# Kernel tuning notes

Measured on AMD Instinct MI355X. Metric: run time of the kernel, lower is better.

## Reference

```python
import jax, jax.numpy as jnp
import numpy as np

WS = 16        # window size
SHIFT = 8      # shift for odd blocks
DEPTH = 2      # number of stacked blocks
HEADS = 8
EPS = 1e-5


def window_partition(x, ws):
    # x: (B,H,W,C) -> (B*nw, ws*ws, C)
    B, H, W, C = x.shape
    x = x.reshape(B, H // ws, ws, W // ws, ws, C).transpose(0, 1, 3, 2, 4, 5)
    return x.reshape(-1, ws * ws, C)


def window_reverse(wins, ws, H, W):
    B = wins.shape[0] // ((H // ws) * (W // ws))
    x = wins.reshape(B, H // ws, W // ws, ws, ws, -1).transpose(0, 1, 3, 2, 4, 5)
    return x.reshape(B, H, W, -1)


def layernorm(x, g, b):
    m = jnp.mean(x, axis=-1, keepdims=True)
    v = jnp.mean(jnp.square(x - m), axis=-1, keepdims=True)
    return (x - m) * jax.lax.rsqrt(v + EPS) * g + b


def _make_rpi(ws):
    # Swin relative position index, shape (ws*ws, ws*ws), int32
    coords = np.stack(np.meshgrid(np.arange(ws), np.arange(ws), indexing='ij'))  # (2,ws,ws)
    coords = coords.reshape(2, -1)
    rel = coords[:, :, None] - coords[:, None, :]  # (2, n, n)
    rel = rel + (ws - 1)
    rpi = rel[0] * (2 * ws - 1) + rel[1]
    return jnp.asarray(rpi, dtype=jnp.int32)


def _make_attn_mask(H, W, ws, shift):
    # Swin shifted-window mask, shape (nw, n, n) with 0 / -100
    img = np.zeros((1, H, W, 1), dtype=np.float32)
    cnt = 0
    slices = (slice(0, -ws), slice(-ws, -shift), slice(-shift, None))
    for hs in slices:
        for wsl in slices:
            img[:, hs, wsl, :] = cnt
            cnt += 1
    mw = window_partition(jnp.asarray(img), ws).reshape(-1, ws * ws)  # (nw, n)
    mask = mw[:, None, :] - mw[:, :, None]
    return jnp.where(mask != 0, jnp.float32(-100.0), jnp.float32(0.0))


def setup_inputs() -> dict:
    key = jax.random.key(0)
    ks = jax.random.split(key, 8)
    B, H, W, C = 8, 64, 64, 256
    hid = 4 * C
    d = DEPTH
    s = 0.02
    inp = {
        'x':      jax.random.normal(ks[0], (B, H, W, C), jnp.float32),
        'ln1_g':  jnp.ones((d, C), jnp.float32),
        'ln1_b':  jnp.zeros((d, C), jnp.float32),
        'qkv_w':  jax.random.normal(ks[1], (d, C, 3 * C), jnp.float32) * s,
        'qkv_b':  jnp.zeros((d, 3 * C), jnp.float32),
        'rpb':    jax.random.normal(ks[2], (d, (2 * WS - 1) ** 2, HEADS), jnp.float32) * s,
        'proj_w': jax.random.normal(ks[3], (d, C, C), jnp.float32) * s,
        'proj_b': jnp.zeros((d, C), jnp.float32),
        'ln2_g':  jnp.ones((d, C), jnp.float32),
        'ln2_b':  jnp.zeros((d, C), jnp.float32),
        'fc1_w':  jax.random.normal(ks[4], (d, C, hid), jnp.float32) * s,
        'fc1_b':  jnp.zeros((d, hid), jnp.float32),
        'fc2_w':  jax.random.normal(ks[5], (d, hid, C), jnp.float32) * s,
        'fc2_b':  jnp.zeros((d, C), jnp.float32),
        'attn_mask': _make_attn_mask(H, W, WS, SHIFT),
        'rpi':    _make_rpi(WS),
    }
    return inp


def _forward(x, ln1_g, ln1_b, qkv_w, qkv_b, rpb, proj_w, proj_b,
             ln2_g, ln2_b, fc1_w, fc1_b, fc2_w, fc2_b, attn_mask, rpi):
    B, H, W, C = x.shape
    n = WS * WS
    hd = C // HEADS
    scale = jnp.float32(hd) ** -0.5
    for i in range(DEPTH):
        shift = SHIFT if (i % 2 == 1) else 0
        shortcut = x
        y = layernorm(x, ln1_g[i], ln1_b[i])
        if shift:
            y = jnp.roll(y, (-shift, -shift), axis=(1, 2))
        wins = window_partition(y, WS)                      # (b_, n, C)
        b_ = wins.shape[0]
        qkv = wins @ qkv_w[i] + qkv_b[i]
        qkv = qkv.reshape(b_, n, 3, HEADS, hd).transpose(2, 0, 3, 1, 4)
        q, k, v = qkv[0] * scale, qkv[1], qkv[2]            # (b_,h,n,hd)
        attn = jnp.einsum('bhnd,bhmd->bhnm', q, k)          # (b_,h,n,n)
        bias = rpb[i][rpi.reshape(-1)].reshape(n, n, HEADS).transpose(2, 0, 1)
        attn = attn + bias[None]
        if shift:
            nw = attn_mask.shape[0]
            attn = attn.reshape(B, nw, HEADS, n, n) + attn_mask[None, :, None]
            attn = attn.reshape(b_, HEADS, n, n)
        attn = jax.nn.softmax(attn, axis=-1)
        out = jnp.einsum('bhnm,bhmd->bhnd', attn, v)
        out = out.transpose(0, 2, 1, 3).reshape(b_, n, C)
        out = out @ proj_w[i] + proj_b[i]
        y = window_reverse(out, WS, H, W)
        if shift:
            y = jnp.roll(y, (shift, shift), axis=(1, 2))
        x = shortcut + y
        z = layernorm(x, ln2_g[i], ln2_b[i])
        z = jax.nn.gelu(z @ fc1_w[i] + fc1_b[i], approximate=False)
        z = z @ fc2_w[i] + fc2_b[i]
        x = x + z
    return x


def reference(x, ln1_g, ln1_b, qkv_w, qkv_b, rpb, proj_w, proj_b,
              ln2_g, ln2_b, fc1_w, fc1_b, fc2_w, fc2_b, attn_mask, rpi):
    return _forward(x, ln1_g, ln1_b, qkv_w, qkv_b, rpb, proj_w, proj_b,
                    ln2_g, ln2_b, fc1_w, fc1_b, fc2_w, fc2_b, attn_mask, rpi)
```

## Files before the change

kernel.cpp:

```cpp
#include <hip/hip_runtime.h>

typedef unsigned short u16;
typedef __attribute__((ext_vector_type(8))) short short8;
typedef __attribute__((ext_vector_type(4))) float f32x4;

#define GLDS16(gp, sp) __builtin_amdgcn_global_load_lds( \
    (const __attribute__((address_space(1))) void*)(gp),  \
    (__attribute__((address_space(3))) void*)(sp), 16, 0, 0)

__device__ __forceinline__ u16 f2bf(float f) {
  union { float f; unsigned u; } x; x.f = f;
  unsigned r = (x.u + 0x7fffu + ((x.u >> 16) & 1u)) >> 16;
  return (u16)r;
}
__device__ __forceinline__ float bf2f(u16 v) {
  union { unsigned u; float f; } x; x.u = ((unsigned)v) << 16; return x.f;
}
__device__ __forceinline__ unsigned cvt_pk_bf16(float lo, float hi) {
  unsigned r;
  asm("v_cvt_pk_bf16_f32 %0, %1, %2" : "=v"(r) : "v"(lo), "v"(hi));
  return r;
}
__device__ __forceinline__ float gelu_t(float v) {
  float i = v * (1.f + 0.044715f * v * v);
  float e = __expf(-1.5957691216057308f * i);
  return v * __builtin_amdgcn_rcpf(1.f + e);
}

__global__ __launch_bounds__(256) void wswizB(const float* __restrict__ W,
                                              u16* __restrict__ Wf, int K, int N) {
  int tid = blockIdx.x * 256 + threadIdx.x;
  int Kt = K >> 5, Nt = N >> 4;
  int per = Nt * Kt * 64;
  if (tid >= 2 * per) return;
  int l = tid >= per;
  int rem = tid - l * per;
  int nb = rem / (Kt * 64);
  int rem2 = rem - nb * Kt * 64;
  int ks = rem2 >> 6, lane = rem2 & 63;
  int n = nb * 16 + (lane & 15);
  u16 o[8];
  #pragma unroll
  for (int e = 0; e < 8; ++e) {
    int k = ks * 32 + ((lane >> 4) << 3) + e;
    o[e] = f2bf(W[((size_t)l * K + k) * N + n]);
  }
  *(uint4*)(Wf + ((size_t)tid << 3)) = *(uint4*)o;
}

__global__ __launch_bounds__(256) void wswiz1(const float* __restrict__ W,
                                              u16* __restrict__ Wf) {
  int tid = blockIdx.x * 256 + threadIdx.x;
  int lane = tid & 63, nt = (tid >> 6) & 7, ks = (tid >> 9) & 7,
      hc = (tid >> 12) & 7, l = tid >> 15;
  int n = hc * 128 + nt * 16 + (lane & 15);
  u16 o[8];
  #pragma unroll
  for (int e = 0; e < 8; ++e) {
    int k = ks * 32 + ((lane >> 4) << 3) + e;
    o[e] = f2bf(W[((size_t)l * 256 + k) * 1024 + n]);
  }
  *(uint4*)(Wf + ((size_t)tid << 3)) = *(uint4*)o;
}

__global__ __launch_bounds__(256) void wswiz2(const float* __restrict__ W,
                                              u16* __restrict__ Wf) {
  int tid = blockIdx.x * 256 + threadIdx.x;
  int lane = tid & 63, nt = (tid >> 6) & 15, ks = (tid >> 10) & 3,
      hc = (tid >> 12) & 7, l = tid >> 15;
  int n = nt * 16 + (lane & 15);
  u16 o[8];
  #pragma unroll
  for (int e = 0; e < 8; ++e) {
    int k = hc * 128 + ks * 32 + ((lane >> 4) << 3) + e;
    o[e] = f2bf(W[((size_t)l * 1024 + k) * 256 + n]);
  }
  *(uint4*)(Wf + ((size_t)tid << 3)) = *(uint4*)o;
}

__global__ __launch_bounds__(256) void bias_gb(const float* __restrict__ rpb,
                                               const int* __restrict__ rpi,
                                               u16* __restrict__ biasb) {
  int tid = blockIdx.x * 256 + threadIdx.x;
  if (tid >= 131072) return;
  int l = tid >> 16, cid = tid & 65535;
  int lane = cid & 63, k = (cid >> 6) & 7, mslot = (cid >> 9) & 15, h = cid >> 13;
  u16 o[8];
  #pragma unroll
  for (int e = 0; e < 8; ++e) {
    int nt = 2 * k + (e >> 2), r = e & 3;
    int i = mslot * 16 + ((lane >> 4) << 2) + r;
    int j = nt * 16 + (lane & 15);
    int idx = rpi[i * 256 + j];
    o[e] = f2bf(rpb[((size_t)l * 961 + idx) * 8 + h]);
  }
  *(uint4*)(biasb + ((size_t)tid << 3)) = *(uint4*)o;
}

__global__ __launch_bounds__(256) void ln_part(const float* __restrict__ x,
                                               const float* __restrict__ g,
                                               const float* __restrict__ b,
                                               u16* __restrict__ out, int shift) {
  int wv = threadIdx.x >> 6, lane = threadIdx.x & 63;
  int wtok = blockIdx.x * 4 + wv;
  int w = wtok >> 8, t = wtok & 255;
  int bimg = w >> 4, wi = w & 15;
  int ph = (((wi >> 2) << 4) + (t >> 4) + shift) & 63;
  int pw = (((wi & 3) << 4) + (t & 15) + shift) & 63;
  const float4 v = *(const float4*)(x + ((size_t)((bimg * 64 + ph) * 64 + pw)) * 256 + lane * 4);
  float s = v.x + v.y + v.z + v.w;
  float sq = v.x * v.x + v.y * v.y + v.z * v.z + v.w * v.w;
  #pragma unroll
  for (int m = 1; m < 64; m <<= 1) { s += __shfl_xor(s, m, 64); sq += __shfl_xor(sq, m, 64); }
  float mean = s * (1.f / 256.f);
  float var = sq * (1.f / 256.f) - mean * mean;
  float rs = rsqrtf(var + 1e-5f);
  float4 gg = *(const float4*)(g + lane * 4);
  float4 bb = *(const float4*)(b + lane * 4);
  uint2 pk;
  pk.x = cvt_pk_bf16((v.x - mean) * rs * gg.x + bb.x,
                     (v.y - mean) * rs * gg.y + bb.y);
  pk.y = cvt_pk_bf16((v.z - mean) * rs * gg.z + bb.z,
                     (v.w - mean) * rs * gg.w + bb.w);
  *(uint2*)(out + (size_t)wtok * 256 + lane * 4) = pk;
}

struct EpiParams {
  const float* bias;
  u16* obf;
  float* of32;
  const float* resid;
  int shift;
  float qscale;
};

__global__ __launch_bounds__(512, 2) void gemm_fk2(const u16* __restrict__ A,
                                                   const u16* __restrict__ Wf,
                                                   int N, EpiParams ep) {
  __shared__ u16 As[8][128][32];
  int tid = threadIdx.x;
  int n0 = blockIdx.x * 256, m0 = blockIdx.y * 128;
  int wv = tid >> 6, lane = tid & 63, quad = lane >> 4, l15 = lane & 15;
  int wm = wv & 1, wn = wv >> 1;

  #pragma unroll
  for (int i = 0; i < 8; ++i) {
    int c = i * 512 + tid;
    int kb = c >> 9, rc = c & 511;
    int row = rc >> 2, kc = (rc & 3) * 8;
    GLDS16(A + (size_t)(m0 + row) * 256 + kb * 32 + kc, &As[kb][row][kc]);
  }
  __syncthreads();

  f32x4 acc[4][4] = {};
  #pragma unroll
  for (int kb = 0; kb < 8; ++kb) {
    short8 bf[4];
    #pragma unroll
    for (int nt = 0; nt < 4; ++nt) {
      size_t ntile = (size_t)(blockIdx.x * 16 + wn * 4 + nt);
      bf[nt] = *(const short8*)(Wf + ((ntile * 8 + kb) * 64 + lane) * 8);
    }
    #pragma unroll
    for (int mt = 0; mt < 4; ++mt) {
      short8 af = *(const short8*)&As[kb][wm * 64 + mt * 16 + l15][quad * 8];
      #pragma unroll
      for (int nt = 0; nt < 4; ++nt)
        acc[mt][nt] = __builtin_amdgcn_mfma_f32_16x16x32_bf16(af, bf[nt], acc[mt][nt], 0, 0, 0);
    }
  }

  #pragma unroll
  for (int mt = 0; mt < 4; ++mt) {
    #pragma unroll
    for (int nt = 0; nt < 4; ++nt) {
      #pragma unroll
      for (int r = 0; r < 4; ++r) {
        int grow = m0 + wm * 64 + mt * 16 + quad * 4 + r;
        int gcol = n0 + wn * 64 + nt * 16 + l15;
        float v = acc[mt][nt][r] + ep.bias[gcol];
        if (gcol < 256) v *= ep.qscale;
        ep.obf[(size_t)grow * N + gcol] = f2bf(v);
      }
    }
  }
}

template <int EPI>
__global__ __launch_bounds__(512, 2) void gemm_fk(const u16* __restrict__ A,
                                                  const u16* __restrict__ Wf,
                                                  int N, EpiParams ep) {
  __shared__ u16 As[8][128][32];
  int tid = threadIdx.x;
  int n0 = blockIdx.x * 128, m0 = blockIdx.y * 128;
  int wv = tid >> 6, lane = tid & 63, quad = lane >> 4, l15 = lane & 15;
  int wm = wv & 1, wn = wv >> 1;

  #pragma unroll
  for (int i = 0; i < 8; ++i) {
    int c = i * 512 + tid;
    int kb = c >> 9, rc = c & 511;
    int row = rc >> 2, kc = (rc & 3) * 8;
    GLDS16(A + (size_t)(m0 + row) * 256 + kb * 32 + kc, &As[kb][row][kc]);
  }
  __syncthreads();

  f32x4 acc[4][2] = {};
  #pragma unroll
  for (int kb = 0; kb < 8; ++kb) {
    short8 bf[2];
    #pragma unroll
    for (int nt = 0; nt < 2; ++nt) {
      size_t ntile = (size_t)(blockIdx.x * 8 + wn * 2 + nt);
      bf[nt] = *(const short8*)(Wf + ((ntile * 8 + kb) * 64 + lane) * 8);
    }
    #pragma unroll
    for (int mt = 0; mt < 4; ++mt) {
      short8 af = *(const short8*)&As[kb][wm * 64 + mt * 16 + l15][quad * 8];
      #pragma unroll
      for (int nt = 0; nt < 2; ++nt)
        acc[mt][nt] = __builtin_amdgcn_mfma_f32_16x16x32_bf16(af, bf[nt], acc[mt][nt], 0, 0, 0);
    }
  }

  #pragma unroll
  for (int mt = 0; mt < 4; ++mt) {
    #pragma unroll
    for (int nt = 0; nt < 2; ++nt) {
      #pragma unroll
      for (int r = 0; r < 4; ++r) {
        int grow = m0 + wm * 64 + mt * 16 + quad * 4 + r;
        int gcol = n0 + wn * 32 + nt * 16 + l15;
        float v = acc[mt][nt][r] + ep.bias[gcol];
        if constexpr (EPI == 0) {
          if (gcol < 256) v *= ep.qscale;
          ep.obf[(size_t)grow * N + gcol] = f2bf(v);
        } else {
          int w_ = grow >> 8, t = grow & 255, wi = w_ & 15;
          int ph = (((wi >> 2) << 4) + (t >> 4) + ep.shift) & 63;
          int pw = (((wi & 3) << 4) + (t & 15) + ep.shift) & 63;
          size_t pix = (size_t)(((w_ >> 4) * 64 + ph) * 64 + pw);
          ep.of32[pix * 256 + gcol] = ep.resid[pix * 256 + gcol] + v;
        }
      }
    }
  }
}

__global__ __launch_bounds__(512, 4) void fused_mlp(const float* __restrict__ xin,
                                                    const float* __restrict__ g,
                                                    const float* __restrict__ b,
                                                    const u16* __restrict__ W1f,
                                                    const u16* __restrict__ W2f,
                                                    const float* __restrict__ b1p,
                                                    const float* __restrict__ b2p,
                                                    float* __restrict__ out) {
  __shared__ u16 Zs[64 * 264];
  __shared__ u16 Hs[2][64 * 136];
  int tid = threadIdx.x, wv = tid >> 6, lane = tid & 63;
  int quad = lane >> 4, l15 = lane & 15;
  int m0 = blockIdx.x * 64;

  float4 gg = *(const float4*)(g + lane * 4);
  float4 bb = *(const float4*)(b + lane * 4);
  #pragma unroll
  for (int rr = 0; rr < 8; ++rr) {
    int row = wv * 8 + rr;
    const float4 v = *(const float4*)(xin + (size_t)(m0 + row) * 256 + lane * 4);
    float s = v.x + v.y + v.z + v.w;
    float sq = v.x * v.x + v.y * v.y + v.z * v.z + v.w * v.w;
    #pragma unroll
    for (int m = 1; m < 64; m <<= 1) { s += __shfl_xor(s, m, 64); sq += __shfl_xor(sq, m, 64); }
    float mean = s * (1.f / 256.f);
    float var = sq * (1.f / 256.f) - mean * mean;
    float rs = rsqrtf(var + 1e-5f);
    uint2 pk;
    pk.x = cvt_pk_bf16((v.x - mean) * rs * gg.x + bb.x,
                       (v.y - mean) * rs * gg.y + bb.y);
    pk.y = cvt_pk_bf16((v.z - mean) * rs * gg.z + bb.z,
                       (v.w - mean) * rs * gg.w + bb.w);
    *(uint2*)&Zs[row * 264 + lane * 4] = pk;
  }
  __syncthreads();

  f32x4 acc2[4][2];
  #pragma unroll
  for (int nt = 0; nt < 2; ++nt) {
    float4 b2 = *(const float4*)(b2p + wv * 32 + nt * 16 + quad * 4);
    #pragma unroll
    for (int mt = 0; mt < 4; ++mt) {
      acc2[mt][nt][0] = b2.x; acc2[mt][nt][1] = b2.y;
      acc2[mt][nt][2] = b2.z; acc2[mt][nt][3] = b2.w;
    }
  }

  f32x4 acc1a[4], acc1b[4];

  {
    float4 b1a = *(const float4*)(b1p + 0 * 128 + wv * 16 + quad * 4);
    float4 b1b = *(const float4*)(b1p + 1 * 128 + wv * 16 + quad * 4);
    #pragma unroll
    for (int mt = 0; mt < 4; ++mt) {
      acc1a[mt][0] = b1a.x; acc1a[mt][1] = b1a.y; acc1a[mt][2] = b1a.z; acc1a[mt][3] = b1a.w;
      acc1b[mt][0] = b1b.x; acc1b[mt][1] = b1b.y; acc1b[mt][2] = b1b.z; acc1b[mt][3] = b1b.w;
    }
    #pragma unroll
    for (int ks = 0; ks < 8; ++ks) {
      short8 w1a = *(const short8*)(W1f + ((((size_t)0 * 8 + ks) * 8 + wv) * 64 + lane) * 8);
      short8 w1b = *(const short8*)(W1f + ((((size_t)1 * 8 + ks) * 8 + wv) * 64 + lane) * 8);
      #pragma unroll
      for (int mt = 0; mt < 4; ++mt) {
        short8 zf = *(const short8*)&Zs[(mt * 16 + l15) * 264 + ks * 32 + quad * 8];
        acc1a[mt] = __builtin_amdgcn_mfma_f32_16x16x32_bf16(w1a, zf, acc1a[mt], 0, 0, 0);
        acc1b[mt] = __builtin_amdgcn_mfma_f32_16x16x32_bf16(w1b, zf, acc1b[mt], 0, 0, 0);
      }
    }
    #pragma unroll
    for (int mt = 0; mt < 4; ++mt) {
      uint2 pa, pb;
      pa.x = cvt_pk_bf16(gelu_t(acc1a[mt][0]), gelu_t(acc1a[mt][1]));
      pa.y = cvt_pk_bf16(gelu_t(acc1a[mt][2]), gelu_t(acc1a[mt][3]));
      pb.x = cvt_pk_bf16(gelu_t(acc1b[mt][0]), gelu_t(acc1b[mt][1]));
      pb.y = cvt_pk_bf16(gelu_t(acc1b[mt][2]), gelu_t(acc1b[mt][3]));
      int ha = (mt * 16 + l15) * 136 + wv * 16 + quad * 4;
      *(uint2*)&Hs[0][ha] = pa;
      *(uint2*)&Hs[1][ha] = pb;
    }
  }
  __syncthreads();

  for (int hp = 1; hp < 4; ++hp) {
    int hcA = 2 * hp, hcB = 2 * hp + 1, hcP = 2 * (hp - 1);
    float4 b1a = *(const float4*)(b1p + hcA * 128 + wv * 16 + quad * 4);
    float4 b1b = *(const float4*)(b1p + hcB * 128 + wv * 16 + quad * 4);
    #pragma unroll
    for (int mt = 0; mt < 4; ++mt) {
      acc1a[mt][0] = b1a.x; acc1a[mt][1] = b1a.y; acc1a[mt][2] = b1a.z; acc1a[mt][3] = b1a.w;
      acc1b[mt][0] = b1b.x; acc1b[mt][1] = b1b.y; acc1b[mt][2] = b1b.z; acc1b[mt][3] = b1b.w;
    }
    #pragma unroll
    for (int ks = 0; ks < 8; ++ks) {
      const int buf = ks >> 2, ks2 = ks & 3;
      short8 w1a = *(const short8*)(W1f + ((((size_t)hcA * 8 + ks) * 8 + wv) * 64 + lane) * 8);
      short8 w1b = *(const short8*)(W1f + ((((size_t)hcB * 8 + ks) * 8 + wv) * 64 + lane) * 8);
      short8 w20 = *(const short8*)(W2f + ((((size_t)(hcP + buf) * 4 + ks2) * 16 + wv * 2 + 0) * 64 + lane) * 8);
      short8 w21 = *(const short8*)(W2f + ((((size_t)(hcP + buf) * 4 + ks2) * 16 + wv * 2 + 1) * 64 + lane) * 8);
      #pragma unroll
      for (int mt = 0; mt < 4; ++mt) {
        short8 zf = *(const short8*)&Zs[(mt * 16 + l15) * 264 + ks * 32 + quad * 8];
        short8 hf = *(const short8*)&Hs[buf][(mt * 16 + l15) * 136 + ks2 * 32 + quad * 8];
        acc1a[mt] = __builtin_amdgcn_mfma_f32_16x16x32_bf16(w1a, zf, acc1a[mt], 0, 0, 0);
        acc1b[mt] = __builtin_amdgcn_mfma_f32_16x16x32_bf16(w1b, zf, acc1b[mt], 0, 0, 0);
        acc2[mt][0] = __builtin_amdgcn_mfma_f32_16x16x32_bf16(w20, hf, acc2[mt][0], 0, 0, 0);
        acc2[mt][1] = __builtin_amdgcn_mfma_f32_16x16x32_bf16(w21, hf, acc2[mt][1], 0, 0, 0);
      }
    }
    uint2 pka[4], pkb[4];
    #pragma unroll
    for (int mt = 0; mt < 4; ++mt) {
      pka[mt].x = cvt_pk_bf16(gelu_t(acc1a[mt][0]), gelu_t(acc1a[mt][1]));
      pka[mt].y = cvt_pk_bf16(gelu_t(acc1a[mt][2]), gelu_t(acc1a[mt][3]));
      pkb[mt].x = cvt_pk_bf16(gelu_t(acc1b[mt][0]), gelu_t(acc1b[mt][1]));
      pkb[mt].y = cvt_pk_bf16(gelu_t(acc1b[mt][2]), gelu_t(acc1b[mt][3]));
    }
    __syncthreads();
    #pragma unroll
    for (int mt = 0; mt < 4; ++mt) {
      int ha = (mt * 16 + l15) * 136 + wv * 16 + quad * 4;
      *(uint2*)&Hs[0][ha] = pka[mt];
      *(uint2*)&Hs[1][ha] = pkb[mt];
    }
    __syncthreads();
  }

  #pragma unroll
  for (int ks = 0; ks < 8; ++ks) {
    const int buf = ks >> 2, ks2 = ks & 3;
    short8 w20 = *(const short8*)(W2f + ((((size_t)(6 + buf) * 4 + ks2) * 16 + wv * 2 + 0) * 64 + lane) * 8);
    short8 w21 = *(const short8*)(W2f + ((((size_t)(6 + buf) * 4 + ks2) * 16 + wv * 2 + 1) * 64 + lane) * 8);
    #pragma unroll
    for (int mt = 0; mt < 4; ++mt) {
      short8 hf = *(const short8*)&Hs[buf][(mt * 16 + l15) * 136 + ks2 * 32 + quad * 8];
      acc2[mt][0] = __builtin_amdgcn_mfma_f32_16x16x32_bf16(w20, hf, acc2[mt][0], 0, 0, 0);
      acc2[mt][1] = __builtin_amdgcn_mfma_f32_16x16x32_bf16(w21, hf, acc2[mt][1], 0, 0, 0);
    }
  }

  #pragma unroll
  for (int mt = 0; mt < 4; ++mt) {
    #pragma unroll
    for (int nt = 0; nt < 2; ++nt) {
      size_t idx = (size_t)(m0 + mt * 16 + l15) * 256 + wv * 32 + nt * 16 + quad * 4;
      float4 r = *(const float4*)(xin + idx);
      float4 o;
      o.x = r.x + acc2[mt][nt][0];
      o.y = r.y + acc2[mt][nt][1];
      o.z = r.z + acc2[mt][nt][2];
      o.w = r.w + acc2[mt][nt][3];
      *(float4*)(out + idx) = o;
    }
  }
}

__global__ __launch_bounds__(256, 4) void attn_v3(const u16* __restrict__ qkv,
                                                  const u16* __restrict__ biasb,
                                                  int layer, u16* __restrict__ aout) {
  __shared__ u16 Klds[256 * 32];
  __shared__ u16 Vt[32 * 264];
  __shared__ u16 Plds[4][16 * 40];
  int bid = blockIdx.x;
  int lw = ((bid & 7) << 7) | (bid >> 3);
  int w = lw >> 3, h = lw & 7;
  int tid = threadIdx.x;

  {
    const uint4* kp = (const uint4*)(qkv + ((size_t)(w * 256 + tid)) * 768 + 256 + h * 32);
    uint4* kd = (uint4*)&Klds[tid * 32];
    kd[0] = kp[0]; kd[1] = kp[1]; kd[2] = kp[2]; kd[3] = kp[3];
    const uint4* vp = (const uint4*)(qkv + ((size_t)(w * 256 + tid)) * 768 + 512 + h * 32);
    u16 vt[32];
    *(uint4*)&vt[0]  = vp[0];
    *(uint4*)&vt[8]  = vp[1];
    *(uint4*)&vt[16] = vp[2];
    *(uint4*)&vt[24] = vp[3];
    #pragma unroll
    for (int d = 0; d < 32; ++d) Vt[d * 264 + tid] = vt[d];
  }
  __syncthreads();

  int wv = tid >> 6, lane = tid & 63, quad = lane >> 4, l15 = lane & 15;
  int wi = w & 15, wr = wi >> 2, wc = wi & 3;
  const bool masked = (layer != 0) && (wr == 3 || wc == 3);
  int rcj = (wc == 3) ? (l15 < 8 ? 1 : 2) : 0;

  #pragma unroll
  for (int mt = 0; mt < 4; ++mt) {
    int mslot = wv * 4 + mt;
    int m0 = mslot * 16;
    short8 aq = *(const short8*)(qkv + ((size_t)(w * 256 + m0 + l15)) * 768 + h * 32 + quad * 8);
    const u16* bmt = biasb + ((size_t)layer << 19) + ((size_t)h << 16) + (size_t)mslot * 4096;
    f32x4 c[16];
    #pragma unroll
    for (int k = 0; k < 8; ++k) {
      short8 bv = *(const short8*)(bmt + k * 512 + lane * 8);
      #pragma unroll
      for (int r = 0; r < 4; ++r) {
        c[2 * k][r]     = bf2f((u16)bv[r]);
        c[2 * k + 1][r] = bf2f((u16)bv[4 + r]);
      }
    }
    #pragma unroll
    for (int nt = 0; nt < 16; ++nt) {
      short8 bk = *(const short8*)&Klds[(nt * 16 + l15) * 32 + quad * 8];
      c[nt] = __builtin_amdgcn_mfma_f32_16x16x32_bf16(aq, bk, c[nt], 0, 0, 0);
    }
    if (masked) {
      int regi = ((wr == 3) ? (mslot < 8 ? 1 : 2) : 0) * 3 +
                 ((wc == 3) ? (quad < 2 ? 1 : 2) : 0);
      #pragma unroll
      for (int nt = 0; nt < 16; ++nt) {
        int regj = ((wr == 3) ? (nt < 8 ? 1 : 2) : 0) * 3 + rcj;
        float madd = (regi != regj) ? -100.f : 0.f;
        #pragma unroll
        for (int r = 0; r < 4; ++r) c[nt][r] += madd;
      }
    }
    float pm[4] = {-1e30f, -1e30f, -1e30f, -1e30f};
    #pragma unroll
    for (int nt = 0; nt < 16; ++nt)
      #pragma unroll
      for (int r = 0; r < 4; ++r) pm[r] = fmaxf(pm[r], c[nt][r]);
    #pragma unroll
    for (int r = 0; r < 4; ++r) {
      pm[r] = fmaxf(pm[r], __shfl_xor(pm[r], 1, 64));
      pm[r] = fmaxf(pm[r], __shfl_xor(pm[r], 2, 64));
      pm[r] = fmaxf(pm[r], __shfl_xor(pm[r], 4, 64));
      pm[r] = fmaxf(pm[r], __shfl_xor(pm[r], 8, 64));
    }
    float psum[4] = {0.f, 0.f, 0.f, 0.f};
    #pragma unroll
    for (int nt = 0; nt < 16; ++nt)
      #pragma unroll
      for (int r = 0; r < 4; ++r) {
        float e = __expf(c[nt][r] - pm[r]);
        c[nt][r] = e;
        psum[r] += e;
      }
    #pragma unroll
    for (int r = 0; r < 4; ++r) {
      psum[r] += __shfl_xor(psum[r], 1, 64);
      psum[r] += __shfl_xor(psum[r], 2, 64);
      psum[r] += __shfl_xor(psum[r], 4, 64);
      psum[r] += __shfl_xor(psum[r], 8, 64);
    }
    f32x4 o0 = {0.f, 0.f, 0.f, 0.f}, o1 = {0.f, 0.f, 0.f, 0.f};
    #pragma unroll
    for (int kk = 0; kk < 8; ++kk) {
      #pragma unroll
      for (int r = 0; r < 4; ++r) {
        Plds[wv][(quad * 4 + r) * 40 + l15] = f2bf(c[2 * kk][r]);
        Plds[wv][(quad * 4 + r) * 40 + 16 + l15] = f2bf(c[2 * kk + 1][r]);
      }
      short8 ap = *(const short8*)&Plds[wv][l15 * 40 + quad * 8];
      short8 bv0 = *(const short8*)&Vt[l15 * 264 + kk * 32 + quad * 8];
      short8 bv1 = *(const short8*)&Vt[(16 + l15) * 264 + kk * 32 + quad * 8];
      o0 = __builtin_amdgcn_mfma_f32_16x16x32_bf16(ap, bv0, o0, 0, 0, 0);
      o1 = __builtin_amdgcn_mfma_f32_16x16x32_bf16(ap, bv1, o1, 0, 0, 0);
    }
    #pragma unroll
    for (int r = 0; r < 4; ++r) {
      float inv = 1.f / psum[r];
      size_t row = (size_t)(w * 256 + m0 + quad * 4 + r);
      aout[row * 256 + h * 32 + l15] = f2bf(o0[r] * inv);
      aout[row * 256 + h * 32 + 16 + l15] = f2bf(o1[r] * inv);
    }
  }
}

extern "C" void kernel_launch(void* const* d_in, const int* in_sizes, int n_in,
                              void* d_out, int out_size, void* d_ws, size_t ws_size,
                              hipStream_t stream) {
  const float* x      = (const float*)d_in[0];
  const float* ln1_g  = (const float*)d_in[1];
  const float* ln1_b  = (const float*)d_in[2];
  const float* qkv_w  = (const float*)d_in[3];
  const float* qkv_b  = (const float*)d_in[4];
  const float* rpb    = (const float*)d_in[5];
  const float* proj_w = (const float*)d_in[6];
  const float* proj_b = (const float*)d_in[7];
  const float* ln2_g  = (const float*)d_in[8];
  const float* ln2_b  = (const float*)d_in[9];
  const float* fc1_w  = (const float*)d_in[10];
  const float* fc1_b  = (const float*)d_in[11];
  const float* fc2_w  = (const float*)d_in[12];
  const float* fc2_b  = (const float*)d_in[13];
  const int*   rpi    = (const int*)d_in[15];

  char* ws = (char*)d_ws;
  size_t off = 0;
  auto alloc = [&](size_t bytes) { void* p = ws + off; off += (bytes + 255) & ~(size_t)255; return p; };
  float* x_cur   = (float*)alloc((size_t)32768 * 256 * 4);
  u16* sbuf      = (u16*)alloc((size_t)32768 * 256 * 2);
  u16* qkvb      = (u16*)alloc((size_t)32768 * 768 * 2);
  u16* biasb     = (u16*)alloc((size_t)2 * 8 * 65536 * 2);
  u16* qkvF      = (u16*)alloc((size_t)2 * 196608 * 2);
  u16* projF     = (u16*)alloc((size_t)2 * 65536 * 2);
  u16* W1f       = (u16*)alloc((size_t)2 * 262144 * 2);
  u16* W2f       = (u16*)alloc((size_t)2 * 262144 * 2);

  wswizB<<<192, 256, 0, stream>>>(qkv_w, qkvF, 256, 768);
  wswizB<<<64, 256, 0, stream>>>(proj_w, projF, 256, 256);
  wswiz1<<<256, 256, 0, stream>>>(fc1_w, W1f);
  wswiz2<<<256, 256, 0, stream>>>(fc2_w, W2f);
  bias_gb<<<512, 256, 0, stream>>>(rpb, rpi, biasb);

  for (int i = 0; i < 2; ++i) {
    int shift = i ? 8 : 0;
    const float* xin = i ? x_cur : x;

    ln_part<<<8192, 256, 0, stream>>>(xin, ln1_g + i * 256, ln1_b + i * 256, sbuf, shift);

    EpiParams ep{};
    ep.bias = qkv_b + i * 768; ep.obf = qkvb; ep.qscale = 0.17677669529663687f;
    gemm_fk2<<<dim3(3, 256), 512, 0, stream>>>(sbuf, qkvF + (size_t)i * 196608, 768, ep);

    attn_v3<<<1024, 256, 0, stream>>>(qkvb, biasb, i, sbuf);

    ep = EpiParams{};
    ep.bias = proj_b + i * 256; ep.of32 = x_cur; ep.resid = xin; ep.shift = shift;
    gemm_fk<2><<<dim3(2, 256), 512, 0, stream>>>(sbuf, projF + (size_t)i * 65536, 256, ep);

    fused_mlp<<<512, 512, 0, stream>>>(x_cur, ln2_g + i * 256, ln2_b + i * 256,
                                       W1f + (size_t)i * 262144, W2f + (size_t)i * 262144,
                                       fc1_b + i * 1024, fc2_b + i * 256,
                                       (i == 1) ? (float*)d_out : x_cur);
  }
}
```

Before: 422.4 us.

## Serialize fc1 and fc2 phases per hidden chunk instead of software pipelining

Replaces the software-pipelined MLP loop, where fc1 of chunk hp overlapped with fc2 of chunk hp-1, with a simple per-chunk sequence: fc1 plus GELU into shared memory, a barrier, fc2 from shared memory, then another barrier. This lowers register pressure because fc1 and fc2 accumulators and weight fragments are no longer live at the same time, which may allow better occupancy or less spilling. In exchange it gives up the overlap of the two GEMM phases and keeps two barriers per chunk.

```diff
diff --git a/kernel.cpp b/kernel.cpp
--- a/kernel.cpp
+++ b/kernel.cpp
@@ -294,20 +294,22 @@
     }
   }
 
-  f32x4 acc1a[4], acc1b[4];
-
-  {
-    float4 b1a = *(const float4*)(b1p + 0 * 128 + wv * 16 + quad * 4);
-    float4 b1b = *(const float4*)(b1p + 1 * 128 + wv * 16 + quad * 4);
-    #pragma unroll
-    for (int mt = 0; mt < 4; ++mt) {
-      acc1a[mt][0] = b1a.x; acc1a[mt][1] = b1a.y; acc1a[mt][2] = b1a.z; acc1a[mt][3] = b1a.w;
-      acc1b[mt][0] = b1b.x; acc1b[mt][1] = b1b.y; acc1b[mt][2] = b1b.z; acc1b[mt][3] = b1b.w;
+  for (int hp = 0; hp < 4; ++hp) {
+    int hcA = 2 * hp, hcB = 2 * hp + 1;
+    f32x4 acc1a[4], acc1b[4];
+    {
+      float4 b1a = *(const float4*)(b1p + hcA * 128 + wv * 16 + quad * 4);
+      float4 b1b = *(const float4*)(b1p + hcB * 128 + wv * 16 + quad * 4);
+      #pragma unroll
+      for (int mt = 0; mt < 4; ++mt) {
+        acc1a[mt][0] = b1a.x; acc1a[mt][1] = b1a.y; acc1a[mt][2] = b1a.z; acc1a[mt][3] = b1a.w;
+        acc1b[mt][0] = b1b.x; acc1b[mt][1] = b1b.y; acc1b[mt][2] = b1b.z; acc1b[mt][3] = b1b.w;
+      }
     }
     #pragma unroll
     for (int ks = 0; ks < 8; ++ks) {
-      short8 w1a = *(const short8*)(W1f + ((((size_t)0 * 8 + ks) * 8 + wv) * 64 + lane) * 8);
-      short8 w1b = *(const short8*)(W1f + ((((size_t)1 * 8 + ks) * 8 + wv) * 64 + lane) * 8);
+      short8 w1a = *(const short8*)(W1f + ((((size_t)hcA * 8 + ks) * 8 + wv) * 64 + lane) * 8);
+      short8 w1b = *(const short8*)(W1f + ((((size_t)hcB * 8 + ks) * 8 + wv) * 64 + lane) * 8);
       #pragma unroll
       for (int mt = 0; mt < 4; ++mt) {
         short8 zf = *(const short8*)&Zs[(mt * 16 + l15) * 264 + ks * 32 + quad * 8];
@@ -326,64 +328,23 @@
       *(uint2*)&Hs[0][ha] = pa;
       *(uint2*)&Hs[1][ha] = pb;
     }
-  }
-  __syncthreads();
-
-  for (int hp = 1; hp < 4; ++hp) {
-    int hcA = 2 * hp, hcB = 2 * hp + 1, hcP = 2 * (hp - 1);
-    float4 b1a = *(const float4*)(b1p + hcA * 128 + wv * 16 + quad * 4);
-    float4 b1b = *(const float4*)(b1p + hcB * 128 + wv * 16 + quad * 4);
-    #pragma unroll
-    for (int mt = 0; mt < 4; ++mt) {
-      acc1a[mt][0] = b1a.x; acc1a[mt][1] = b1a.y; acc1a[mt][2] = b1a.z; acc1a[mt][3] = b1a.w;
-      acc1b[mt][0] = b1b.x; acc1b[mt][1] = b1b.y; acc1b[mt][2] = b1b.z; acc1b[mt][3] = b1b.w;
-    }
-    #pragma unroll
-    for (int ks = 0; ks < 8; ++ks) {
-      const int buf = ks >> 2, ks2 = ks & 3;
-      short8 w1a = *(const short8*)(W1f + ((((size_t)hcA * 8 + ks) * 8 + wv) * 64 + lane) * 8);
-      short8 w1b = *(const short8*)(W1f + ((((size_t)hcB * 8 + ks) * 8 + wv) * 64 + lane) * 8);
-      short8 w20 = *(const short8*)(W2f + ((((size_t)(hcP + buf) * 4 + ks2) * 16 + wv * 2 + 0) * 64 + lane) * 8);
-      short8 w21 = *(const short8*)(W2f + ((((size_t)(hcP + buf) * 4 + ks2) * 16 + wv * 2 + 1) * 64 + lane) * 8);
-      #pragma unroll
-      for (int mt = 0; mt < 4; ++mt) {
-        short8 zf = *(const short8*)&Zs[(mt * 16 + l15) * 264 + ks * 32 + quad * 8];
-        short8 hf = *(const short8*)&Hs[buf][(mt * 16 + l15) * 136 + ks2 * 32 + quad * 8];
-        acc1a[mt] = __builtin_amdgcn_mfma_f32_16x16x32_bf16(w1a, zf, acc1a[mt], 0, 0, 0);
-        acc1b[mt] = __builtin_amdgcn_mfma_f32_16x16x32_bf16(w1b, zf, acc1b[mt], 0, 0, 0);
-        acc2[mt][0] = __builtin_amdgcn_mfma_f32_16x16x32_bf16(w20, hf, acc2[mt][0], 0, 0, 0);
-        acc2[mt][1] = __builtin_amdgcn_mfma_f32_16x16x32_bf16(w21, hf, acc2[mt][1], 0, 0, 0);
-      }
-    }
-    uint2 pka[4], pkb[4];
-    #pragma unroll
-    for (int mt = 0; mt < 4; ++mt) {
-      pka[mt].x = cvt_pk_bf16(gelu_t(acc1a[mt][0]), gelu_t(acc1a[mt][1]));
-      pka[mt].y = cvt_pk_bf16(gelu_t(acc1a[mt][2]), gelu_t(acc1a[mt][3]));
-      pkb[mt].x = cvt_pk_bf16(gelu_t(acc1b[mt][0]), gelu_t(acc1b[mt][1]));
-      pkb[mt].y = cvt_pk_bf16(gelu_t(acc1b[mt][2]), gelu_t(acc1b[mt][3]));
-    }
     __syncthreads();
     #pragma unroll
-    for (int mt = 0; mt < 4; ++mt) {
-      int ha = (mt * 16 + l15) * 136 + wv * 16 + quad * 4;
-      *(uint2*)&Hs[0][ha] = pka[mt];
-      *(uint2*)&Hs[1][ha] = pkb[mt];
+    for (int buf = 0; buf < 2; ++buf) {
+      int hc = 2 * hp + buf;
+      #pragma unroll
+      for (int ks2 = 0; ks2 < 4; ++ks2) {
+        short8 w20 = *(const short8*)(W2f + ((((size_t)hc * 4 + ks2) * 16 + wv * 2 + 0) * 64 + lane) * 8);
+        short8 w21 = *(const short8*)(W2f + ((((size_t)hc * 4 + ks2) * 16 + wv * 2 + 1) * 64 + lane) * 8);
+        #pragma unroll
+        for (int mt = 0; mt < 4; ++mt) {
+          short8 hf = *(const short8*)&Hs[buf][(mt * 16 + l15) * 136 + ks2 * 32 + quad * 8];
+          acc2[mt][0] = __builtin_amdgcn_mfma_f32_16x16x32_bf16(w20, hf, acc2[mt][0], 0, 0, 0);
+          acc2[mt][1] = __builtin_amdgcn_mfma_f32_16x16x32_bf16(w21, hf, acc2[mt][1], 0, 0, 0);
+        }
+      }
     }
     __syncthreads();
-  }
-
-  #pragma unroll
-  for (int ks = 0; ks < 8; ++ks) {
-    const int buf = ks >> 2, ks2 = ks & 3;
-    short8 w20 = *(const short8*)(W2f + ((((size_t)(6 + buf) * 4 + ks2) * 16 + wv * 2 + 0) * 64 + lane) * 8);
-    short8 w21 = *(const short8*)(W2f + ((((size_t)(6 + buf) * 4 + ks2) * 16 + wv * 2 + 1) * 64 + lane) * 8);
-    #pragma unroll
-    for (int mt = 0; mt < 4; ++mt) {
-      short8 hf = *(const short8*)&Hs[buf][(mt * 16 + l15) * 136 + ks2 * 32 + quad * 8];
-      acc2[mt][0] = __builtin_amdgcn_mfma_f32_16x16x32_bf16(w20, hf, acc2[mt][0], 0, 0, 0);
-      acc2[mt][1] = __builtin_amdgcn_mfma_f32_16x16x32_bf16(w21, hf, acc2[mt][1], 0, 0, 0);
-    }
   }
 
   #pragma unroll
```

Result: faster. 403.6 us (-4.4%).
